# Kernel tuning notes

Measured on AMD Instinct MI355X. Metric: run time of the kernel, lower is better.

Reference implementation:

```python
import jax, jax.numpy as jnp
import numpy as np

B, T, H, NEX, ED = 65536, 20, 10, 13, 3

def _p(k, shape):
    return (jax.random.normal(k, shape, jnp.float32) * 0.1)

def setup_inputs() -> dict:
    key = jax.random.key(0)
    ks = jax.random.split(key, 24)
    e = jax.random.randint(ks[0], (B, T), 0, NEX, dtype=jnp.int32)
    f = jax.random.normal(ks[1], (B, T, 3), jnp.float32)
    emb = _p(ks[2], (NEX, ED)).at[0].set(0.0)  # row 0 zeroed as in torch init
    feat_w = _p(ks[3], (3, 3))
    feat_b = _p(ks[4], (3,))
    d = {"e": e, "f": f, "emb": emb, "feat_w": feat_w, "feat_b": feat_b}
    i = 5
    for layer, insz in ((0, 6), (1, 2 * H)):
        for sfx in ("", "r"):
            d[f"w_ih_l{layer}{sfx}"] = _p(ks[i], (4 * H, insz)); i += 1
            d[f"w_hh_l{layer}{sfx}"] = _p(ks[i], (4 * H, H)); i += 1
            d[f"b_ih_l{layer}{sfx}"] = _p(ks[i], (4 * H,)); i += 1
            d[f"b_hh_l{layer}{sfx}"] = _p(ks[i], (4 * H,)); i += 1
    return d

def _lstm_dir(x, w_ih, w_hh, b_ih, b_hh, reverse):
    # x: (B, T, I) -> hidden sequence (B, T, H). PyTorch gate order: i, f, g, o.
    xs = jnp.swapaxes(x, 0, 1)                      # (T, B, I)
    pre = xs @ w_ih.T + (b_ih + b_hh)               # input contribution, (T, B, 4H)
    def step(carry, p):
        h, c = carry
        g = p + h @ w_hh.T
        i, fg, gg, o = jnp.split(g, 4, axis=-1)
        c = jax.nn.sigmoid(fg) * c + jax.nn.sigmoid(i) * jnp.tanh(gg)
        h = jax.nn.sigmoid(o) * jnp.tanh(c)
        return (h, c), h
    nb = x.shape[0]
    init = (jnp.zeros((nb, H), x.dtype), jnp.zeros((nb, H), x.dtype))
    _, hs = jax.lax.scan(step, init, pre, reverse=reverse)
    return jnp.swapaxes(hs, 0, 1)                   # (B, T, H)

def _bilstm_layer(x, pf, pb):
    hf = _lstm_dir(x, *pf, reverse=False)
    hb = _lstm_dir(x, *pb, reverse=True)
    return jnp.concatenate([hf, hb], axis=-1)       # (B, T, 2H)

def reference(e, f, emb, feat_w, feat_b,
              w_ih_l0, w_hh_l0, b_ih_l0, b_hh_l0,
              w_ih_l0r, w_hh_l0r, b_ih_l0r, b_hh_l0r,
              w_ih_l1, w_hh_l1, b_ih_l1, b_hh_l1,
              w_ih_l1r, w_hh_l1r, b_ih_l1r, b_hh_l1r):
    ev = emb[e]                                     # (B, T, 3)
    f3 = f.reshape(-1, T, 3)
    mask = (f3[:, :, 1] != 0).astype(f.dtype)       # (B, T)
    fv = f3 @ feat_w.T + feat_b                     # (B, T, 3)
    x = jnp.concatenate([ev, fv], axis=2)           # (B, T, 6)
    x = _bilstm_layer(x, (w_ih_l0, w_hh_l0, b_ih_l0, b_hh_l0),
                         (w_ih_l0r, w_hh_l0r, b_ih_l0r, b_hh_l0r))
    x = _bilstm_layer(x, (w_ih_l1, w_hh_l1, b_ih_l1, b_hh_l1),
                         (w_ih_l1r, w_hh_l1r, b_ih_l1r, b_hh_l1r))
    ipe = jax.nn.relu(x[:, :, -1] * mask)           # last channel = backward dir unit H-1
    total = ipe.sum(axis=1, keepdims=True)          # (B, 1)
    return (total, ipe)
```

## Files before the change

### kernel.cpp

```cpp
#include <hip/hip_runtime.h>

#define BB 65536
#define TT 20
#define NBLK 2048

#define WS_WGT 0
#define WS_HF0 4096
#define PK1 0x00003C00u

#define LOG2E  1.442695041f
#define LOG2E2 2.885390082f

typedef unsigned u32;
typedef __fp16 f16x8 __attribute__((ext_vector_type(8)));
typedef float   f32x16 __attribute__((ext_vector_type(16)));
typedef u32     u32x4 __attribute__((ext_vector_type(4)));
typedef __fp16  h2v   __attribute__((ext_vector_type(2)));

__device__ __forceinline__ u32 pk_h16(float a, float b) {
    h2v v = __builtin_amdgcn_cvt_pkrtz(a, b);
    return __builtin_bit_cast(u32, v);
}
__device__ __forceinline__ f32x16 MFMA(u32x4 a, u32x4 b, f32x16 c) {
    return __builtin_amdgcn_mfma_f32_32x32x16_f16(
        __builtin_bit_cast(f16x8, a), __builtin_bit_cast(f16x8, b), c, 0, 0, 0);
}

__device__ __forceinline__ void unit_cr(float ai, float af, float ag, float ao,
                                        float* c, float* h) {
    float pi = __builtin_amdgcn_exp2f(-LOG2E * ai);
    float pf = __builtin_amdgcn_exp2f(-LOG2E * af);
    float q  = __builtin_amdgcn_exp2f(LOG2E2 * ag);
    float fv = __builtin_amdgcn_rcpf(1.0f + pf);
    float ig = (q - 1.0f) * __builtin_amdgcn_rcpf((1.0f + pi) * (q + 1.0f));
    float cv = fmaf(fv, *c, ig);
    *c = cv;
    float po = __builtin_amdgcn_exp2f(-LOG2E * ao);
    float qc = __builtin_amdgcn_exp2f(LOG2E2 * cv);
    *h = (qc - 1.0f) * __builtin_amdgcn_rcpf((1.0f + po) * (qc + 1.0f));
}

__device__ __forceinline__ u32x4 pack_h(const float* h, bool hi, int xaddr, u32 b3) {
    u32 send = hi ? pk_h16(h[3], h[4]) : __float_as_uint(h[4]);
    u32 recv = (u32)__builtin_amdgcn_ds_bpermute(xaddr, (int)send);
    u32 lo0 = pk_h16(h[0], h[1]), lo1 = pk_h16(h[2], h[3]);
    u32 hi0 = pk_h16(__uint_as_float(recv), h[0]);
    u32 hi1 = pk_h16(h[1], h[2]);
    u32x4 b;
    b[0] = hi ? hi0 : lo0;
    b[1] = hi ? hi1 : lo1;
    b[2] = hi ? 0u : recv;
    b[3] = b3;
    return b;
}

__device__ __forceinline__ void cell_update5(const f32x16 a0, const f32x16 a1,
                                             float* c, float* h) {
#pragma unroll
    for (int v = 0; v < 4; ++v)
        unit_cr(a0[v], a0[4 + v], a0[8 + v], a0[12 + v], &c[v], &h[v]);
    unit_cr(a1[0], a1[1], a1[2], a1[3], &c[4], &h[4]);
}

__device__ __forceinline__ int inv_pi(int row) {
    if (row < 32) { int q = row >> 3, rem = row & 7; return q * 10 + 5 * (rem >> 2) + (rem & 3); }
    if (row < 40) { int lo = row - 32; return (lo & 3) * 10 + 5 * (lo >> 2) + 4; }
    return -1;
}

__global__ __launch_bounds__(256)
void prep_mfma(
    const float* __restrict__ wih0, const float* __restrict__ whh0,
    const float* __restrict__ bih0, const float* __restrict__ bhh0,
    const float* __restrict__ wih0r,const float* __restrict__ whh0r,
    const float* __restrict__ bih0r,const float* __restrict__ bhh0r,
    const float* __restrict__ wih1r,const float* __restrict__ whh1r,
    const float* __restrict__ bih1r,const float* __restrict__ bhh1r,
    u32* __restrict__ ws)
{
    for (int gid = threadIdx.x; gid < 14 * 64 * 4; gid += 256) {
        int fid = gid >> 8, l = (gid >> 2) & 63, j = gid & 3;
        int g = l >> 5;
        int tile, chunk;
        if (fid < 8) { tile = (fid >> 1) & 1; chunk = fid & 1; }
        else         { int q = fid - 8; tile = q / 3; chunk = q % 3; }
        int row = tile * 32 + (l & 31);
        int orow = inv_pi(row);
        int kb = (j >> 1) * 8 + 4 * g + (j & 1) * 2;
        float v[2] = {0.f, 0.f};
        if (orow >= 0) {
#pragma unroll
            for (int s = 0; s < 2; ++s) {
                int k = kb + s;
                float val = 0.f;
                if (fid < 8) {
                    bool bwd = fid >= 4;
                    if (chunk == 0) {
                        if (k < 6)       val = (bwd ? wih0r : wih0)[orow * 6 + k];
                        else if (k == 6) val = (bwd ? bih0r[orow] + bhh0r[orow]
                                                    : bih0[orow] + bhh0[orow]);
                    } else {
                        if (k < 10)      val = (bwd ? whh0r : whh0)[orow * 10 + k];
                    }
                } else {
                    if (chunk == 0)      { if (k < 10) val = wih1r[orow * 20 + k]; }
                    else if (chunk == 1) { if (k < 10) val = wih1r[orow * 20 + 10 + k]; }
                    else {
                        if (k < 10)      val = whh1r[orow * 10 + k];
                        else if (k == 10) val = bih1r[orow] + bhh1r[orow];
                    }
                }
                v[s] = val;
            }
        }
        ws[WS_WGT + (fid * 64 + l) * 4 + j] = pk_h16(v[0], v[1]);
    }
}

template<bool WS> struct Lds {
    u32   x[TT][3][32];
    float m[TT][32];
    u32   hf[WS ? 1 : TT][160];
};

template<bool WS>
__global__ __launch_bounds__(64)
void bilstm_mfma(
    const int*   __restrict__ eidx, const float* __restrict__ f,
    const float* __restrict__ emb,  const float* __restrict__ fw,
    const float* __restrict__ fb,
    const u32* __restrict__ wsr, u32* __restrict__ ghf,
    float* __restrict__ out)
{
    __shared__ Lds<WS> lds;
    const int  lane = threadIdx.x;
    const int  e    = lane & 31;
    const bool hi   = lane >= 32;
    const int  wid  = blockIdx.x;
    const int  b0   = wid * 32;
    const int  xaddr = (lane ^ 32) << 2;
    u32* hfp = ghf + (size_t)wid * TT * 160;

    {
        float fw0=fw[0],fw1=fw[1],fw2=fw[2],fw3=fw[3],fw4=fw[4];
        float fw5=fw[5],fw6=fw[6],fw7=fw[7],fw8=fw[8];
        float fb0=fb[0],fb1=fb[1],fb2=fb[2];
#pragma unroll 1
        for (int it = 0; it < 10; ++it) {
            int idx = lane + it * 64;
            int ee = idx / 20, t = idx - ee * 20;
            int gi = (b0 + ee) * TT + t;
            float f0 = f[gi * 3], f1 = f[gi * 3 + 1], f2v = f[gi * 3 + 2];
            int ei = eidx[gi] * 3;
            float x0 = emb[ei], x1 = emb[ei + 1], x2 = emb[ei + 2];
            float x3 = fmaf(fw0, f0, fmaf(fw1, f1, fmaf(fw2, f2v, fb0)));
            float x4 = fmaf(fw3, f0, fmaf(fw4, f1, fmaf(fw5, f2v, fb1)));
            float x5 = fmaf(fw6, f0, fmaf(fw7, f1, fmaf(fw8, f2v, fb2)));
            lds.x[t][0][ee] = pk_h16(x0, x1);
            lds.x[t][1][ee] = pk_h16(x2, x3);
            lds.x[t][2][ee] = pk_h16(x4, x5);
            lds.m[t][ee]    = (f1 != 0.f) ? 1.f : 0.f;
        }
    }

    const u32x4* wv = (const u32x4*)wsr;
    const f32x16 zf = {};

    {
        u32x4 wf0 = wv[0 * 64 + lane], wf1 = wv[1 * 64 + lane];
        u32x4 wf2 = wv[2 * 64 + lane], wf3 = wv[3 * 64 + lane];
        float cf[5] = {0,0,0,0,0}, hv[5] = {0,0,0,0,0};
        u32x4 bx0;
        {
            u32 x01 = lds.x[0][0][e], x23 = lds.x[0][1][e], x45 = lds.x[0][2][e];
            bx0[0] = hi ? x45 : x01; bx0[1] = hi ? PK1 : x23; bx0[2] = 0u; bx0[3] = 0u;
        }
        f32x16 a0x = MFMA(wf0, bx0, zf);
        f32x16 a1x = MFMA(wf2, bx0, zf);
#pragma unroll 1
        for (int t = 0; t < TT; ++t) {
            u32x4 bh = pack_h(hv, hi, xaddr, 0u);
            f32x16 a0 = MFMA(wf1, bh, a0x);
            f32x16 a1 = MFMA(wf3, bh, a1x);
            if (t + 1 < TT) {
                u32 x01 = lds.x[t+1][0][e], x23 = lds.x[t+1][1][e], x45 = lds.x[t+1][2][e];
                u32x4 bx; bx[0] = hi ? x45 : x01; bx[1] = hi ? PK1 : x23; bx[2] = 0u; bx[3] = 0u;
                a0x = MFMA(wf0, bx, zf);
                a1x = MFMA(wf2, bx, zf);
            }
            cell_update5(a0, a1, cf, hv);
            u32x4 st = pack_h(hv, hi, xaddr, 0u);
            if (WS) {
                *(uint2*)(hfp + t * 160 + lane * 2) = make_uint2(st[0], st[1]);
                if (!hi) hfp[t * 160 + 128 + e] = st[2];
            } else {
                lds.hf[t][lane * 2] = st[0]; lds.hf[t][lane * 2 + 1] = st[1];
                if (!hi) lds.hf[t][128 + e] = st[2];
            }
        }
    }

    {
        u32x4 wb0 = wv[4 * 64 + lane], wb1 = wv[5 * 64 + lane];
        u32x4 wb2 = wv[6 * 64 + lane], wb3 = wv[7 * 64 + lane];
        u32x4 wB0 = wv[8 * 64 + lane], wB1 = wv[9 * 64 + lane], wB2 = wv[10 * 64 + lane];
        u32x4 wB3 = wv[11 * 64 + lane], wB4 = wv[12 * 64 + lane], wB5 = wv[13 * 64 + lane];
        float cb[5] = {0,0,0,0,0}, hbv[5] = {0,0,0,0,0};
        float cc[5] = {0,0,0,0,0}, h1v[5] = {0,0,0,0,0};
        float tot = 0.f;

        {
            u32 x01 = lds.x[TT-1][0][e], x23 = lds.x[TT-1][1][e], x45 = lds.x[TT-1][2][e];
            u32x4 bx; bx[0] = hi ? x45 : x01; bx[1] = hi ? PK1 : x23; bx[2] = 0u; bx[3] = 0u;
            f32x16 a0 = MFMA(wb0, bx, zf);
            f32x16 a1 = MFMA(wb2, bx, zf);
            cell_update5(a0, a1, cb, hbv);
        }
        uint2 cur2; u32 curw;
        if (WS) { cur2 = *(const uint2*)(hfp + (TT-1) * 160 + lane * 2);
                  curw = hfp[(TT-1) * 160 + 128 + e]; }
        else    { cur2 = make_uint2(lds.hf[TT-1][lane * 2], lds.hf[TT-1][lane * 2 + 1]);
                  curw = lds.hf[TT-1][128 + e]; }

#pragma unroll 1
        for (int t = TT - 1; t >= 1; --t) {
            uint2 nxt2; u32 nxtw;
            if (WS) { nxt2 = *(const uint2*)(hfp + (t-1) * 160 + lane * 2);
                      nxtw = hfp[(t-1) * 160 + 128 + e]; }
            else    { nxt2 = make_uint2(lds.hf[t-1][lane * 2], lds.hf[t-1][lane * 2 + 1]);
                      nxtw = lds.hf[t-1][128 + e]; }
            u32x4 shared = pack_h(hbv, hi, xaddr, 0u);
            u32x4 bh1    = pack_h(h1v, hi, xaddr, hi ? 0u : PK1);
            u32x4 bhf; bhf[0] = cur2.x; bhf[1] = cur2.y; bhf[2] = hi ? 0u : curw; bhf[3] = 0u;
            f32x16 B0 = MFMA(wB0, bhf, zf); B0 = MFMA(wB1, shared, B0); B0 = MFMA(wB2, bh1, B0);
            f32x16 B1 = MFMA(wB3, bhf, zf); B1 = MFMA(wB4, shared, B1); B1 = MFMA(wB5, bh1, B1);
            u32 x01 = lds.x[t-1][0][e], x23 = lds.x[t-1][1][e], x45 = lds.x[t-1][2][e];
            u32x4 bx; bx[0] = hi ? x45 : x01; bx[1] = hi ? PK1 : x23; bx[2] = 0u; bx[3] = 0u;
            f32x16 A0 = MFMA(wb0, bx, zf); A0 = MFMA(wb1, shared, A0);
            f32x16 A1 = MFMA(wb2, bx, zf); A1 = MFMA(wb3, shared, A1);
            cell_update5(B0, B1, cc, h1v);
            if (hi) {
                float ip = fmaxf(h1v[4] * lds.m[t][e], 0.f);
                out[BB + (b0 + e) * TT + t] = ip;
                tot += ip;
            }
            cell_update5(A0, A1, cb, hbv);
            cur2 = nxt2; curw = nxtw;
        }
        {
            u32x4 shared = pack_h(hbv, hi, xaddr, 0u);
            u32x4 bh1    = pack_h(h1v, hi, xaddr, hi ? 0u : PK1);
            u32x4 bhf; bhf[0] = cur2.x; bhf[1] = cur2.y; bhf[2] = hi ? 0u : curw; bhf[3] = 0u;
            f32x16 B0 = MFMA(wB0, bhf, zf); B0 = MFMA(wB1, shared, B0); B0 = MFMA(wB2, bh1, B0);
            f32x16 B1 = MFMA(wB3, bhf, zf); B1 = MFMA(wB4, shared, B1); B1 = MFMA(wB5, bh1, B1);
            cell_update5(B0, B1, cc, h1v);
            if (hi) {
                float ip = fmaxf(h1v[4] * lds.m[0][e], 0.f);
                out[BB + (b0 + e) * TT + 0] = ip;
                tot += ip;
                out[b0 + e] = tot;
            }
        }
    }
}

extern "C" void kernel_launch(void* const* d_in, const int* in_sizes, int n_in,
                              void* d_out, int out_size, void* d_ws, size_t ws_size,
                              hipStream_t stream) {
    const int*   eidx  = (const int*)  d_in[0];
    const float* f     = (const float*)d_in[1];
    const float* emb   = (const float*)d_in[2];
    const float* fw    = (const float*)d_in[3];
    const float* fb    = (const float*)d_in[4];
    const float* wih0  = (const float*)d_in[5];
    const float* whh0  = (const float*)d_in[6];
    const float* bih0  = (const float*)d_in[7];
    const float* bhh0  = (const float*)d_in[8];
    const float* wih0r = (const float*)d_in[9];
    const float* whh0r = (const float*)d_in[10];
    const float* bih0r = (const float*)d_in[11];
    const float* bhh0r = (const float*)d_in[12];
    const float* wih1r = (const float*)d_in[17];
    const float* whh1r = (const float*)d_in[18];
    const float* bih1r = (const float*)d_in[19];
    const float* bhh1r = (const float*)d_in[20];
    float* out = (float*)d_out;
    u32* ws = (u32*)d_ws;

    hipLaunchKernelGGL(prep_mfma, dim3(1), dim3(256), 0, stream,
                       wih0, whh0, bih0, bhh0, wih0r, whh0r, bih0r, bhh0r,
                       wih1r, whh1r, bih1r, bhh1r, ws);

    const size_t need = (size_t)(WS_HF0 + (size_t)NBLK * TT * 160) * 4;
    dim3 grid(NBLK), block(64);
    if (ws_size >= need) {
        hipLaunchKernelGGL(bilstm_mfma<true>, grid, block, 0, stream,
                           eidx, f, emb, fw, fb, ws, ws + WS_HF0, out);
    } else {
        hipLaunchKernelGGL(bilstm_mfma<false>, grid, block, 0, stream,
                           eidx, f, emb, fw, fb, ws, ws + WS_HF0, out);
    }
}
```

Baseline: 69.94 us.

## Split bidirectional layer 0 into parallel per-direction blocks plus a layer-1 kernel

Layer 0 moves into its own kernel that runs forward and backward directions as separate workgroups (4096 blocks), each writing its hidden-state fragments to workspace. A second kernel then runs the layer-1 backward recurrence by reading both direction buffers. The aim is to double parallelism and shorten the serial dependency chain per block, because the backward layer-0 recurrence no longer sits in the same loop as layer 1. The cost is an extra launch, duplicated input preprocessing, and more global memory traffic for the layer-0 backward states. The first step also skips the MFMA with a zero hidden state.

```diff
diff --git a/kernel.cpp b/kernel.cpp
--- a/kernel.cpp
+++ b/kernel.cpp
@@ -2,10 +2,13 @@
 
 #define BB 65536
 #define TT 20
-#define NBLK 2048
+#define NE 2048
+#define FRAG_T 160
 
 #define WS_WGT 0
 #define WS_HF0 4096
+#define WS_HB0 (WS_HF0 + NE * TT * FRAG_T)
+#define WS_END (WS_HB0 + NE * TT * FRAG_T)
 #define PK1 0x00003C00u
 
 #define LOG2E  1.442695041f
@@ -117,10 +120,137 @@
     }
 }
 
+__global__ __launch_bounds__(64)
+void bilstm_l0(
+    const int*   __restrict__ eidx, const float* __restrict__ f,
+    const float* __restrict__ emb,  const float* __restrict__ fw,
+    const float* __restrict__ fb,
+    const u32* __restrict__ wsr, u32* __restrict__ ghf, u32* __restrict__ ghb)
+{
+    __shared__ u32 xs[TT][3][32];
+    const int  lane = threadIdx.x;
+    const int  e    = lane & 31;
+    const bool hi   = lane >= 32;
+    const int  wid  = blockIdx.x;
+    const int  dir  = wid >> 11;
+    const int  eb   = wid & (NE - 1);
+    const int  b0   = eb * 32;
+    const int  xaddr = (lane ^ 32) << 2;
+
+    {
+        float fw0=fw[0],fw1=fw[1],fw2=fw[2],fw3=fw[3],fw4=fw[4];
+        float fw5=fw[5],fw6=fw[6],fw7=fw[7],fw8=fw[8];
+        float fb0=fb[0],fb1=fb[1],fb2=fb[2];
+#pragma unroll 1
+        for (int it = 0; it < 10; ++it) {
+            int idx = lane + it * 64;
+            int ee = idx / 20, t = idx - ee * 20;
+            int gi = (b0 + ee) * TT + t;
+            float f0 = f[gi * 3], f1 = f[gi * 3 + 1], f2v = f[gi * 3 + 2];
+            int ei = eidx[gi] * 3;
+            float x0 = emb[ei], x1 = emb[ei + 1], x2 = emb[ei + 2];
+            float x3 = fmaf(fw0, f0, fmaf(fw1, f1, fmaf(fw2, f2v, fb0)));
+            float x4 = fmaf(fw3, f0, fmaf(fw4, f1, fmaf(fw5, f2v, fb1)));
+            float x5 = fmaf(fw6, f0, fmaf(fw7, f1, fmaf(fw8, f2v, fb2)));
+            xs[t][0][ee] = pk_h16(x0, x1);
+            xs[t][1][ee] = pk_h16(x2, x3);
+            xs[t][2][ee] = pk_h16(x4, x5);
+        }
+    }
+
+    const u32x4* wv = (const u32x4*)wsr;
+    const f32x16 zf = {};
+    u32* outp = (dir ? ghb : ghf) + (size_t)eb * TT * FRAG_T;
+    const int wbase = dir ? 4 : 0;
+    u32x4 w0 = wv[(wbase + 0) * 64 + lane], w1 = wv[(wbase + 1) * 64 + lane];
+    u32x4 w2 = wv[(wbase + 2) * 64 + lane], w3 = wv[(wbase + 3) * 64 + lane];
+
+    auto BX = [&](int t) {
+        u32 x01 = xs[t][0][e], x23 = xs[t][1][e], x45 = xs[t][2][e];
+        u32x4 b; b[0] = hi ? x45 : x01; b[1] = hi ? PK1 : x23; b[2] = 0u; b[3] = 0u;
+        return b;
+    };
+
+    float cst[5] = {0,0,0,0,0}, hv[5] = {0,0,0,0,0};
+    const int t0 = dir ? TT - 1 : 0;
+    const int dt = dir ? -1 : 1;
+    f32x16 a0x = MFMA(w0, BX(t0), zf);
+    f32x16 a1x = MFMA(w2, BX(t0), zf);
+    u32x4 bh;
+#pragma unroll 1
+    for (int s = 0; s < TT; ++s) {
+        const int t = t0 + s * dt;
+        f32x16 a0 = a0x, a1 = a1x;
+        if (s > 0) { a0 = MFMA(w1, bh, a0); a1 = MFMA(w3, bh, a1); }
+        if (s + 1 < TT) {
+            u32x4 bx = BX(t + dt);
+            a0x = MFMA(w0, bx, zf);
+            a1x = MFMA(w2, bx, zf);
+        }
+        cell_update5(a0, a1, cst, hv);
+        bh = pack_h(hv, hi, xaddr, 0u);
+        *(uint2*)(outp + t * FRAG_T + lane * 2) = make_uint2(bh[0], bh[1]);
+        if (!hi) outp[t * FRAG_T + 128 + e] = bh[2];
+    }
+}
+
+__global__ __launch_bounds__(64)
+void bilstm_cb(
+    const float* __restrict__ f, const u32* __restrict__ wsr,
+    const u32* __restrict__ ghf, const u32* __restrict__ ghb,
+    float* __restrict__ out)
+{
+    const int  lane = threadIdx.x;
+    const int  e    = lane & 31;
+    const bool hi   = lane >= 32;
+    const int  eb   = blockIdx.x;
+    const int  b0   = eb * 32;
+    const int  xaddr = (lane ^ 32) << 2;
+    const u32x4* wv = (const u32x4*)wsr;
+    u32x4 wB0 = wv[8 * 64 + lane],  wB1 = wv[9 * 64 + lane],  wB2 = wv[10 * 64 + lane];
+    u32x4 wB3 = wv[11 * 64 + lane], wB4 = wv[12 * 64 + lane], wB5 = wv[13 * 64 + lane];
+    const u32* hfp = ghf + (size_t)eb * TT * FRAG_T;
+    const u32* hbp = ghb + (size_t)eb * TT * FRAG_T;
+    const f32x16 zf = {};
+    float cc[5] = {0,0,0,0,0}, h1v[5] = {0,0,0,0,0}, tot = 0.f;
+
+    uint2 hf2 = *(const uint2*)(hfp + (TT - 1) * FRAG_T + lane * 2);
+    u32   hfw = hfp[(TT - 1) * FRAG_T + 128 + e];
+    uint2 hb2 = *(const uint2*)(hbp + (TT - 1) * FRAG_T + lane * 2);
+    u32   hbw = hbp[(TT - 1) * FRAG_T + 128 + e];
+    float f1v = f[((b0 + e) * TT + (TT - 1)) * 3 + 1];
+
+#pragma unroll 1
+    for (int t = TT - 1; t >= 0; --t) {
+        u32x4 bhf; bhf[0] = hf2.x; bhf[1] = hf2.y; bhf[2] = hi ? 0u : hfw; bhf[3] = 0u;
+        u32x4 bhb; bhb[0] = hb2.x; bhb[1] = hb2.y; bhb[2] = hi ? 0u : hbw; bhb[3] = 0u;
+        f32x16 B0 = MFMA(wB0, bhf, zf); B0 = MFMA(wB1, bhb, B0);
+        f32x16 B1 = MFMA(wB3, bhf, zf); B1 = MFMA(wB4, bhb, B1);
+        float fcur = f1v;
+        if (t > 0) {
+            hf2 = *(const uint2*)(hfp + (t - 1) * FRAG_T + lane * 2);
+            hfw = hfp[(t - 1) * FRAG_T + 128 + e];
+            hb2 = *(const uint2*)(hbp + (t - 1) * FRAG_T + lane * 2);
+            hbw = hbp[(t - 1) * FRAG_T + 128 + e];
+            f1v = f[((b0 + e) * TT + (t - 1)) * 3 + 1];
+        }
+        u32x4 bh1 = pack_h(h1v, hi, xaddr, hi ? 0u : PK1);
+        B0 = MFMA(wB2, bh1, B0);
+        B1 = MFMA(wB5, bh1, B1);
+        cell_update5(B0, B1, cc, h1v);
+        if (hi) {
+            float ip = fmaxf(h1v[4] * (fcur != 0.f ? 1.f : 0.f), 0.f);
+            out[BB + (b0 + e) * TT + t] = ip;
+            tot += ip;
+        }
+    }
+    if (hi) out[b0 + e] = tot;
+}
+
 template<bool WS> struct Lds {
     u32   x[TT][3][32];
     float m[TT][32];
-    u32   hf[WS ? 1 : TT][160];
+    u32   hf[WS ? 1 : TT][FRAG_T];
 };
 
 template<bool WS>
@@ -139,7 +269,7 @@
     const int  wid  = blockIdx.x;
     const int  b0   = wid * 32;
     const int  xaddr = (lane ^ 32) << 2;
-    u32* hfp = ghf + (size_t)wid * TT * 160;
+    u32* hfp = ghf + (size_t)wid * TT * FRAG_T;
 
     {
         float fw0=fw[0],fw1=fw[1],fw2=fw[2],fw3=fw[3],fw4=fw[4];
@@ -165,7 +295,6 @@
 
     const u32x4* wv = (const u32x4*)wsr;
     const f32x16 zf = {};
-
     {
         u32x4 wf0 = wv[0 * 64 + lane], wf1 = wv[1 * 64 + lane];
         u32x4 wf2 = wv[2 * 64 + lane], wf3 = wv[3 * 64 + lane];
@@ -177,11 +306,11 @@
         }
         f32x16 a0x = MFMA(wf0, bx0, zf);
         f32x16 a1x = MFMA(wf2, bx0, zf);
+        u32x4 bh;
 #pragma unroll 1
         for (int t = 0; t < TT; ++t) {
-            u32x4 bh = pack_h(hv, hi, xaddr, 0u);
-            f32x16 a0 = MFMA(wf1, bh, a0x);
-            f32x16 a1 = MFMA(wf3, bh, a1x);
+            f32x16 a0 = a0x, a1 = a1x;
+            if (t > 0) { a0 = MFMA(wf1, bh, a0); a1 = MFMA(wf3, bh, a1); }
             if (t + 1 < TT) {
                 u32 x01 = lds.x[t+1][0][e], x23 = lds.x[t+1][1][e], x45 = lds.x[t+1][2][e];
                 u32x4 bx; bx[0] = hi ? x45 : x01; bx[1] = hi ? PK1 : x23; bx[2] = 0u; bx[3] = 0u;
@@ -189,17 +318,16 @@
                 a1x = MFMA(wf2, bx, zf);
             }
             cell_update5(a0, a1, cf, hv);
-            u32x4 st = pack_h(hv, hi, xaddr, 0u);
+            bh = pack_h(hv, hi, xaddr, 0u);
             if (WS) {
-                *(uint2*)(hfp + t * 160 + lane * 2) = make_uint2(st[0], st[1]);
-                if (!hi) hfp[t * 160 + 128 + e] = st[2];
+                *(uint2*)(hfp + t * FRAG_T + lane * 2) = make_uint2(bh[0], bh[1]);
+                if (!hi) hfp[t * FRAG_T + 128 + e] = bh[2];
             } else {
-                lds.hf[t][lane * 2] = st[0]; lds.hf[t][lane * 2 + 1] = st[1];
-                if (!hi) lds.hf[t][128 + e] = st[2];
+                lds.hf[t][lane * 2] = bh[0]; lds.hf[t][lane * 2 + 1] = bh[1];
+                if (!hi) lds.hf[t][128 + e] = bh[2];
             }
         }
     }
-
     {
         u32x4 wb0 = wv[4 * 64 + lane], wb1 = wv[5 * 64 + lane];
         u32x4 wb2 = wv[6 * 64 + lane], wb3 = wv[7 * 64 + lane];
@@ -208,7 +336,6 @@
         float cb[5] = {0,0,0,0,0}, hbv[5] = {0,0,0,0,0};
         float cc[5] = {0,0,0,0,0}, h1v[5] = {0,0,0,0,0};
         float tot = 0.f;
-
         {
             u32 x01 = lds.x[TT-1][0][e], x23 = lds.x[TT-1][1][e], x45 = lds.x[TT-1][2][e];
             u32x4 bx; bx[0] = hi ? x45 : x01; bx[1] = hi ? PK1 : x23; bx[2] = 0u; bx[3] = 0u;
@@ -217,16 +344,15 @@
             cell_update5(a0, a1, cb, hbv);
         }
         uint2 cur2; u32 curw;
-        if (WS) { cur2 = *(const uint2*)(hfp + (TT-1) * 160 + lane * 2);
-                  curw = hfp[(TT-1) * 160 + 128 + e]; }
+        if (WS) { cur2 = *(const uint2*)(hfp + (TT-1) * FRAG_T + lane * 2);
+                  curw = hfp[(TT-1) * FRAG_T + 128 + e]; }
         else    { cur2 = make_uint2(lds.hf[TT-1][lane * 2], lds.hf[TT-1][lane * 2 + 1]);
                   curw = lds.hf[TT-1][128 + e]; }
-
 #pragma unroll 1
         for (int t = TT - 1; t >= 1; --t) {
             uint2 nxt2; u32 nxtw;
-            if (WS) { nxt2 = *(const uint2*)(hfp + (t-1) * 160 + lane * 2);
-                      nxtw = hfp[(t-1) * 160 + 128 + e]; }
+            if (WS) { nxt2 = *(const uint2*)(hfp + (t-1) * FRAG_T + lane * 2);
+                      nxtw = hfp[(t-1) * FRAG_T + 128 + e]; }
             else    { nxt2 = make_uint2(lds.hf[t-1][lane * 2], lds.hf[t-1][lane * 2 + 1]);
                       nxtw = lds.hf[t-1][128 + e]; }
             u32x4 shared = pack_h(hbv, hi, xaddr, 0u);
@@ -291,13 +417,18 @@
                        wih0, whh0, bih0, bhh0, wih0r, whh0r, bih0r, bhh0r,
                        wih1r, whh1r, bih1r, bhh1r, ws);
 
-    const size_t need = (size_t)(WS_HF0 + (size_t)NBLK * TT * 160) * 4;
-    dim3 grid(NBLK), block(64);
-    if (ws_size >= need) {
-        hipLaunchKernelGGL(bilstm_mfma<true>, grid, block, 0, stream,
+    const size_t need_split = (size_t)WS_END * 4;
+    const size_t need_r9    = (size_t)(WS_HF0 + (size_t)NE * TT * FRAG_T) * 4;
+    if (ws_size >= need_split) {
+        hipLaunchKernelGGL(bilstm_l0, dim3(2 * NE), dim3(64), 0, stream,
+                           eidx, f, emb, fw, fb, ws, ws + WS_HF0, ws + WS_HB0);
+        hipLaunchKernelGGL(bilstm_cb, dim3(NE), dim3(64), 0, stream,
+                           f, ws, ws + WS_HF0, ws + WS_HB0, out);
+    } else if (ws_size >= need_r9) {
+        hipLaunchKernelGGL(bilstm_mfma<true>, dim3(NE), dim3(64), 0, stream,
                            eidx, f, emb, fw, fb, ws, ws + WS_HF0, out);
     } else {
-        hipLaunchKernelGGL(bilstm_mfma<false>, grid, block, 0, stream,
+        hipLaunchKernelGGL(bilstm_mfma<false>, dim3(NE), dim3(64), 0, stream,
                            eidx, f, emb, fw, fb, ws, ws + WS_HF0, out);
     }
 }
```

Result: slower. 78.66 us (+12.5%).

## Switch BiLSTM to 16x16x32 MFMA with 16 sequences per wave

Applied to the files above, without the earlier changes.

Replaces the 32x32x16 MFMA kernel (32 sequences per 64-thread block) with a new kernel using 16x16x32 MFMA tiles. Each wave handles 16 sequences and a block holds four waves. Input and recurrent weights are packed into one K=32 operand, so the x and h contributions come from a single MFMA, and h is exchanged through LDS with explicit waitcnt fences instead of bpermute packing. Layer 0 runs the forward and backward directions interleaved in one loop, then layer 1's backward pass reads the stored hidden states. This aims to cut wasted MFMA work on the padded 32-row tiles and raise occupancy, at the cost of an LDS round-trip and fence on every step.

```diff
diff --git a/kernel.cpp b/kernel.cpp
--- a/kernel.cpp
+++ b/kernel.cpp
@@ -2,18 +2,24 @@
 
 #define BB 65536
 #define TT 20
-#define NBLK 2048
-
-#define WS_WGT 0
-#define WS_HF0 4096
-#define PK1 0x00003C00u
+#define NG16 4096
+#define FR_ROW 160
+
+#define WS_AF  0
+#define WS_OLD 2304
+#define WS_FR  8192
+#define PKB 0x00003C00u
 
 #define LOG2E  1.442695041f
 #define LOG2E2 2.885390082f
+
+#define LDS_FENCE() do { asm volatile("s_waitcnt lgkmcnt(0)" ::: "memory"); \
+                         __builtin_amdgcn_sched_barrier(0); } while (0)
 
 typedef unsigned u32;
 typedef __fp16 f16x8 __attribute__((ext_vector_type(8)));
 typedef float   f32x16 __attribute__((ext_vector_type(16)));
+typedef float   f32x4v __attribute__((ext_vector_type(4)));
 typedef u32     u32x4 __attribute__((ext_vector_type(4)));
 typedef __fp16  h2v   __attribute__((ext_vector_type(2)));
 
@@ -21,7 +27,11 @@
     h2v v = __builtin_amdgcn_cvt_pkrtz(a, b);
     return __builtin_bit_cast(u32, v);
 }
-__device__ __forceinline__ f32x16 MFMA(u32x4 a, u32x4 b, f32x16 c) {
+__device__ __forceinline__ f32x4v MFMA16(u32x4 a, u32x4 b, f32x4v c) {
+    return __builtin_amdgcn_mfma_f32_16x16x32_f16(
+        __builtin_bit_cast(f16x8, a), __builtin_bit_cast(f16x8, b), c, 0, 0, 0);
+}
+__device__ __forceinline__ f32x16 MFMA32(u32x4 a, u32x4 b, f32x16 c) {
     return __builtin_amdgcn_mfma_f32_32x32x16_f16(
         __builtin_bit_cast(f16x8, a), __builtin_bit_cast(f16x8, b), c, 0, 0, 0);
 }
@@ -40,20 +50,209 @@
     *h = (qc - 1.0f) * __builtin_amdgcn_rcpf((1.0f + po) * (qc + 1.0f));
 }
 
-__device__ __forceinline__ u32x4 pack_h(const float* h, bool hi, int xaddr, u32 b3) {
+__global__ __launch_bounds__(256)
+void prep16(
+    const float* __restrict__ wih0, const float* __restrict__ whh0,
+    const float* __restrict__ bih0, const float* __restrict__ bhh0,
+    const float* __restrict__ wih0r,const float* __restrict__ whh0r,
+    const float* __restrict__ bih0r,const float* __restrict__ bhh0r,
+    const float* __restrict__ wih1r,const float* __restrict__ whh1r,
+    const float* __restrict__ bih1r,const float* __restrict__ bhh1r,
+    u32* __restrict__ ws)
+{
+    for (int gid = threadIdx.x; gid < 9 * 64 * 4; gid += 256) {
+        int fid = gid >> 8;
+        int ct = fid / 3, T = fid % 3;
+        int l = (gid >> 2) & 63, j = gid & 3;
+        int m = l & 15, qq = l >> 4;
+        int unit = T * 4 + (m >> 2), gate = m & 3;
+        float v[2] = {0.f, 0.f};
+        if (unit <= 9) {
+            int orow = gate * 10 + unit;
+#pragma unroll
+            for (int s = 0; s < 2; ++s) {
+                int k = (j >> 1) * 16 + 4 * qq + (j & 1) * 2 + s;
+                float val = 0.f;
+                if (ct < 2) {
+                    const float* wih = ct ? wih0r : wih0;
+                    const float* whh = ct ? whh0r : whh0;
+                    if (k < 6)            val = wih[orow * 6 + k];
+                    else if (k == 6)      val = ct ? (bih0r[orow] + bhh0r[orow])
+                                               : (bih0[orow] + bhh0[orow]);
+                    else if (k >= 8 && k <= 17) val = whh[orow * 10 + (k - 8)];
+                } else {
+                    if (k < 20)           val = wih1r[orow * 20 + k];
+                    else if (k <= 29)     val = whh1r[orow * 10 + (k - 20)];
+                    else if (k == 30)     val = bih1r[orow] + bhh1r[orow];
+                }
+                v[s] = val;
+            }
+        }
+        ws[WS_AF + (fid * 64 + l) * 4 + j] = pk_h16(v[0], v[1]);
+    }
+}
+
+struct Lds16 {
+    uint2 bx[4][TT][16][2];
+    float m[4][TT][16];
+    unsigned short hx[4][2][16][12];
+    u32   zpad[2];
+};
+
+__global__ __launch_bounds__(256, 4)
+void bilstm16(
+    const int*   __restrict__ eidx, const float* __restrict__ f,
+    const float* __restrict__ emb,  const float* __restrict__ fw,
+    const float* __restrict__ fb,
+    const u32* __restrict__ wsr, u32* __restrict__ fr,
+    float* __restrict__ out)
+{
+    __shared__ Lds16 lds;
+    const int tid  = threadIdx.x;
+    const int lane = tid & 63;
+    const int e    = lane & 15;
+    const int q    = lane >> 4;
+    const int wv   = __builtin_amdgcn_readfirstlane(tid >> 6);
+    const int g    = blockIdx.x * 4 + wv;
+    const int b0   = g * 16;
+    const int be   = e * 24;
+    u32* frp = fr + (size_t)g * TT * FR_ROW;
+
+    {
+        float fw0=fw[0],fw1=fw[1],fw2=fw[2],fw3=fw[3],fw4=fw[4];
+        float fw5=fw[5],fw6=fw[6],fw7=fw[7],fw8=fw[8];
+        float fb0=fb[0],fb1=fb[1],fb2=fb[2];
+#pragma unroll 1
+        for (int it = 0; it < 5; ++it) {
+            int idx = lane + it * 64;
+            int ee = idx / TT, t = idx - ee * TT;
+            int gi = (b0 + ee) * TT + t;
+            float f0 = f[gi * 3], f1 = f[gi * 3 + 1], f2v = f[gi * 3 + 2];
+            int ei = eidx[gi] * 3;
+            float x0 = emb[ei], x1 = emb[ei + 1], x2 = emb[ei + 2];
+            float x3 = fmaf(fw0, f0, fmaf(fw1, f1, fmaf(fw2, f2v, fb0)));
+            float x4 = fmaf(fw3, f0, fmaf(fw4, f1, fmaf(fw5, f2v, fb1)));
+            float x5 = fmaf(fw6, f0, fmaf(fw7, f1, fmaf(fw8, f2v, fb2)));
+            lds.bx[wv][t][ee][0] = make_uint2(pk_h16(x0, x1), pk_h16(x2, x3));
+            lds.bx[wv][t][ee][1] = make_uint2(pk_h16(x4, x5), PKB);
+            lds.m[wv][t][ee]     = (f1 != 0.f) ? 1.f : 0.f;
+        }
+        u32* zz = (u32*)&lds.hx[wv][0][0][0];
+        zz[lane] = 0u; zz[lane + 64] = 0u; zz[lane + 128] = 0u;
+        if (lane < 2) lds.zpad[lane] = 0u;
+    }
+    LDS_FENCE();
+
+    char* bxb  = (char*)&lds.bx[wv][0][e][0];
+    char* hxFb = (char*)&lds.hx[wv][0][0][0];
+    char* hxBb = (char*)&lds.hx[wv][1][0][0];
+    char* hxF  = hxFb + be;
+    char* hxB  = hxBb + be;
+    char* zp   = (char*)lds.zpad;
+    const int uw0 = be + 2 * q, uw1 = be + 8 + 2 * q, uw2 = be + 16 + 2 * q;
+
+    const u32x4* wv4 = (const u32x4*)(wsr + WS_AF);
+    const f32x4v z4 = {};
+
+    {
+        u32x4 F0 = wv4[0 * 64 + lane], F1 = wv4[1 * 64 + lane], F2 = wv4[2 * 64 + lane];
+        u32x4 G0 = wv4[3 * 64 + lane], G1 = wv4[4 * 64 + lane], G2 = wv4[5 * 64 + lane];
+        const char* aF  = (q < 2) ? (bxb + q * 8) : (hxF + (q - 2) * 8);
+        const char* aB  = (q < 2) ? (bxb + q * 8 + 19 * 256) : (hxB + (q - 2) * 8);
+        const char* a2F = (q == 0) ? (hxF + 16) : zp;
+        const char* a2B = (q == 0) ? (hxB + 16) : zp;
+        const int   strA = (q < 2) ? 256 : 0;
+
+        float cF[3] = {0,0,0}, cB[3] = {0,0,0};
+#pragma unroll 1
+        for (int s = 0; s < TT; ++s) {
+            uint2 uF = *(const uint2*)(aF + s * strA);
+            u32   wF = *(const u32*)a2F;
+            u32x4 bf; bf[0] = uF.x; bf[1] = uF.y; bf[2] = wF; bf[3] = 0u;
+            f32x4v A0 = MFMA16(F0, bf, z4), A1 = MFMA16(F1, bf, z4), A2 = MFMA16(F2, bf, z4);
+            uint2 uB = *(const uint2*)(aB - s * strA);
+            u32   wB = *(const u32*)a2B;
+            u32x4 bb; bb[0] = uB.x; bb[1] = uB.y; bb[2] = wB; bb[3] = 0u;
+            f32x4v C0 = MFMA16(G0, bb, z4), C1 = MFMA16(G1, bb, z4), C2 = MFMA16(G2, bb, z4);
+            float hF[3], hB[3];
+            unit_cr(A0[0], A0[1], A0[2], A0[3], &cF[0], &hF[0]);
+            unit_cr(A1[0], A1[1], A1[2], A1[3], &cF[1], &hF[1]);
+            unit_cr(A2[0], A2[1], A2[2], A2[3], &cF[2], &hF[2]);
+            unit_cr(C0[0], C0[1], C0[2], C0[3], &cB[0], &hB[0]);
+            unit_cr(C1[0], C1[1], C1[2], C1[3], &cB[1], &hB[1]);
+            unit_cr(C2[0], C2[1], C2[2], C2[3], &cB[2], &hB[2]);
+            *(__fp16*)(hxFb + uw0) = (__fp16)hF[0];
+            *(__fp16*)(hxFb + uw1) = (__fp16)hF[1];
+            *(__fp16*)(hxFb + uw2) = (__fp16)hF[2];
+            *(__fp16*)(hxBb + uw0) = (__fp16)hB[0];
+            *(__fp16*)(hxBb + uw1) = (__fp16)hB[1];
+            *(__fp16*)(hxBb + uw2) = (__fp16)hB[2];
+            LDS_FENCE();
+            u32* frT = frp + s * FR_ROW;
+            u32* frB = frp + (TT - 1 - s) * FR_ROW;
+            frT[e * 10 + q]     = *(u32*)(hxF + q * 4);
+            frB[e * 10 + 5 + q] = *(u32*)(hxB + q * 4);
+            if (q == 0) {
+                frT[e * 10 + 4] = *(u32*)(hxF + 16);
+                frB[e * 10 + 9] = *(u32*)(hxB + 16);
+            }
+        }
+    }
+
+    {
+        u32x4 H0 = wv4[6 * 64 + lane], H1 = wv4[7 * 64 + lane], H2 = wv4[8 * 64 + lane];
+        u32* hz = (u32*)hxFb;
+        hz[lane] = 0u;
+        if (lane < 32) hz[64 + lane] = 0u;
+        LDS_FENCE();
+        const char* caddr = (q == 0) ? zp : (hxF + (q - 1) * 8);
+        const int loffA = e * 10 + q * 2;
+        const int loffB = e * 10 + 8;
+        float cH[3] = {0,0,0}, tot = 0.f;
+        uint2 La = *(const uint2*)(frp + (TT - 1) * FR_ROW + loffA);
+        uint2 Lb = *(const uint2*)(frp + (TT - 1) * FR_ROW + loffB);
+#pragma unroll 1
+        for (int t = TT - 1; t >= 0; --t) {
+            uint2 C = *(const uint2*)caddr;
+            u32x4 bc;
+            bc[0] = La.x;
+            bc[1] = La.y;
+            bc[2] = (q == 0) ? Lb.x : C.x;
+            bc[3] = (q == 0) ? Lb.y : ((q == 3) ? PKB : C.y);
+            if (t > 0) {
+                La = *(const uint2*)(frp + (t - 1) * FR_ROW + loffA);
+                Lb = *(const uint2*)(frp + (t - 1) * FR_ROW + loffB);
+            }
+            f32x4v D0 = MFMA16(H0, bc, z4), D1 = MFMA16(H1, bc, z4), D2 = MFMA16(H2, bc, z4);
+            float hH[3];
+            unit_cr(D0[0], D0[1], D0[2], D0[3], &cH[0], &hH[0]);
+            unit_cr(D1[0], D1[1], D1[2], D1[3], &cH[1], &hH[1]);
+            unit_cr(D2[0], D2[1], D2[2], D2[3], &cH[2], &hH[2]);
+            *(__fp16*)(hxFb + uw0) = (__fp16)hH[0];
+            *(__fp16*)(hxFb + uw1) = (__fp16)hH[1];
+            *(__fp16*)(hxFb + uw2) = (__fp16)hH[2];
+            LDS_FENCE();
+            if (q == 1) {
+                float ip = fmaxf(hH[2] * lds.m[wv][t][e], 0.f);
+                out[BB + (b0 + e) * TT + t] = ip;
+                tot += ip;
+            }
+        }
+        if (q == 1) out[b0 + e] = tot;
+    }
+}
+
+__device__ __forceinline__ u32x4 pack_h32(const float* h, bool hi, int xaddr, u32 b3) {
     u32 send = hi ? pk_h16(h[3], h[4]) : __float_as_uint(h[4]);
     u32 recv = (u32)__builtin_amdgcn_ds_bpermute(xaddr, (int)send);
     u32 lo0 = pk_h16(h[0], h[1]), lo1 = pk_h16(h[2], h[3]);
     u32 hi0 = pk_h16(__uint_as_float(recv), h[0]);
     u32 hi1 = pk_h16(h[1], h[2]);
     u32x4 b;
-    b[0] = hi ? hi0 : lo0;
-    b[1] = hi ? hi1 : lo1;
-    b[2] = hi ? 0u : recv;
-    b[3] = b3;
+    b[0] = hi ? hi0 : lo0; b[1] = hi ? hi1 : lo1;
+    b[2] = hi ? 0u : recv; b[3] = b3;
     return b;
 }
-
 __device__ __forceinline__ void cell_update5(const f32x16 a0, const f32x16 a1,
                                              float* c, float* h) {
 #pragma unroll
@@ -61,15 +260,13 @@
         unit_cr(a0[v], a0[4 + v], a0[8 + v], a0[12 + v], &c[v], &h[v]);
     unit_cr(a1[0], a1[1], a1[2], a1[3], &c[4], &h[4]);
 }
-
 __device__ __forceinline__ int inv_pi(int row) {
     if (row < 32) { int q = row >> 3, rem = row & 7; return q * 10 + 5 * (rem >> 2) + (rem & 3); }
     if (row < 40) { int lo = row - 32; return (lo & 3) * 10 + 5 * (lo >> 2) + 4; }
     return -1;
 }
-
 __global__ __launch_bounds__(256)
-void prep_mfma(
+void prep_old(
     const float* __restrict__ wih0, const float* __restrict__ whh0,
     const float* __restrict__ bih0, const float* __restrict__ bhh0,
     const float* __restrict__ wih0r,const float* __restrict__ whh0r,
@@ -80,13 +277,13 @@
 {
     for (int gid = threadIdx.x; gid < 14 * 64 * 4; gid += 256) {
         int fid = gid >> 8, l = (gid >> 2) & 63, j = gid & 3;
-        int g = l >> 5;
+        int gq = l >> 5;
         int tile, chunk;
         if (fid < 8) { tile = (fid >> 1) & 1; chunk = fid & 1; }
-        else         { int q = fid - 8; tile = q / 3; chunk = q % 3; }
+        else         { int q2 = fid - 8; tile = q2 / 3; chunk = q2 % 3; }
         int row = tile * 32 + (l & 31);
         int orow = inv_pi(row);
-        int kb = (j >> 1) * 8 + 4 * g + (j & 1) * 2;
+        int kb = (j >> 1) * 8 + 4 * gq + (j & 1) * 2;
         float v[2] = {0.f, 0.f};
         if (orow >= 0) {
 #pragma unroll
@@ -99,48 +296,36 @@
                         if (k < 6)       val = (bwd ? wih0r : wih0)[orow * 6 + k];
                         else if (k == 6) val = (bwd ? bih0r[orow] + bhh0r[orow]
                                                     : bih0[orow] + bhh0[orow]);
-                    } else {
-                        if (k < 10)      val = (bwd ? whh0r : whh0)[orow * 10 + k];
-                    }
+                    } else { if (k < 10) val = (bwd ? whh0r : whh0)[orow * 10 + k]; }
                 } else {
                     if (chunk == 0)      { if (k < 10) val = wih1r[orow * 20 + k]; }
                     else if (chunk == 1) { if (k < 10) val = wih1r[orow * 20 + 10 + k]; }
                     else {
-                        if (k < 10)      val = whh1r[orow * 10 + k];
+                        if (k < 10)       val = whh1r[orow * 10 + k];
                         else if (k == 10) val = bih1r[orow] + bhh1r[orow];
                     }
                 }
                 v[s] = val;
             }
         }
-        ws[WS_WGT + (fid * 64 + l) * 4 + j] = pk_h16(v[0], v[1]);
-    }
-}
-
-template<bool WS> struct Lds {
-    u32   x[TT][3][32];
-    float m[TT][32];
-    u32   hf[WS ? 1 : TT][160];
-};
-
-template<bool WS>
+        ws[WS_OLD + (fid * 64 + l) * 4 + j] = pk_h16(v[0], v[1]);
+    }
+}
+struct LdsFB { u32 x[TT][3][32]; float m[TT][32]; u32 hf[TT][160]; };
 __global__ __launch_bounds__(64)
-void bilstm_mfma(
+void bilstm_fb(
     const int*   __restrict__ eidx, const float* __restrict__ f,
     const float* __restrict__ emb,  const float* __restrict__ fw,
     const float* __restrict__ fb,
-    const u32* __restrict__ wsr, u32* __restrict__ ghf,
-    float* __restrict__ out)
+    const u32* __restrict__ wsr, float* __restrict__ out)
 {
-    __shared__ Lds<WS> lds;
+    __shared__ LdsFB lds;
     const int  lane = threadIdx.x;
     const int  e    = lane & 31;
     const bool hi   = lane >= 32;
     const int  wid  = blockIdx.x;
     const int  b0   = wid * 32;
     const int  xaddr = (lane ^ 32) << 2;
-    u32* hfp = ghf + (size_t)wid * TT * 160;
-
     {
         float fw0=fw[0],fw1=fw[1],fw2=fw[2],fw3=fw[3],fw4=fw[4];
         float fw5=fw[5],fw6=fw[6],fw7=fw[7],fw8=fw[8];
@@ -162,10 +347,8 @@
             lds.m[t][ee]    = (f1 != 0.f) ? 1.f : 0.f;
         }
     }
-
-    const u32x4* wv = (const u32x4*)wsr;
+    const u32x4* wv = (const u32x4*)(wsr + WS_OLD);
     const f32x16 zf = {};
-
     {
         u32x4 wf0 = wv[0 * 64 + lane], wf1 = wv[1 * 64 + lane];
         u32x4 wf2 = wv[2 * 64 + lane], wf3 = wv[3 * 64 + lane];
@@ -173,33 +356,27 @@
         u32x4 bx0;
         {
             u32 x01 = lds.x[0][0][e], x23 = lds.x[0][1][e], x45 = lds.x[0][2][e];
-            bx0[0] = hi ? x45 : x01; bx0[1] = hi ? PK1 : x23; bx0[2] = 0u; bx0[3] = 0u;
-        }
-        f32x16 a0x = MFMA(wf0, bx0, zf);
-        f32x16 a1x = MFMA(wf2, bx0, zf);
+            bx0[0] = hi ? x45 : x01; bx0[1] = hi ? PKB : x23; bx0[2] = 0u; bx0[3] = 0u;
+        }
+        f32x16 a0x = MFMA32(wf0, bx0, zf);
+        f32x16 a1x = MFMA32(wf2, bx0, zf);
+        u32x4 bh;
 #pragma unroll 1
         for (int t = 0; t < TT; ++t) {
-            u32x4 bh = pack_h(hv, hi, xaddr, 0u);
-            f32x16 a0 = MFMA(wf1, bh, a0x);
-            f32x16 a1 = MFMA(wf3, bh, a1x);
+            f32x16 a0 = a0x, a1 = a1x;
+            if (t > 0) { a0 = MFMA32(wf1, bh, a0); a1 = MFMA32(wf3, bh, a1); }
             if (t + 1 < TT) {
                 u32 x01 = lds.x[t+1][0][e], x23 = lds.x[t+1][1][e], x45 = lds.x[t+1][2][e];
-                u32x4 bx; bx[0] = hi ? x45 : x01; bx[1] = hi ? PK1 : x23; bx[2] = 0u; bx[3] = 0u;
-                a0x = MFMA(wf0, bx, zf);
-                a1x = MFMA(wf2, bx, zf);
+                u32x4 bx; bx[0] = hi ? x45 : x01; bx[1] = hi ? PKB : x23; bx[2] = 0u; bx[3] = 0u;
+                a0x = MFMA32(wf0, bx, zf);
+                a1x = MFMA32(wf2, bx, zf);
             }
             cell_update5(a0, a1, cf, hv);
-            u32x4 st = pack_h(hv, hi, xaddr, 0u);
-            if (WS) {
-                *(uint2*)(hfp + t * 160 + lane * 2) = make_uint2(st[0], st[1]);
-                if (!hi) hfp[t * 160 + 128 + e] = st[2];
-            } else {
-                lds.hf[t][lane * 2] = st[0]; lds.hf[t][lane * 2 + 1] = st[1];
-                if (!hi) lds.hf[t][128 + e] = st[2];
-            }
-        }
-    }
-
+            bh = pack_h32(hv, hi, xaddr, 0u);
+            lds.hf[t][lane * 2] = bh[0]; lds.hf[t][lane * 2 + 1] = bh[1];
+            if (!hi) lds.hf[t][128 + e] = bh[2];
+        }
+    }
     {
         u32x4 wb0 = wv[4 * 64 + lane], wb1 = wv[5 * 64 + lane];
         u32x4 wb2 = wv[6 * 64 + lane], wb3 = wv[7 * 64 + lane];
@@ -208,36 +385,28 @@
         float cb[5] = {0,0,0,0,0}, hbv[5] = {0,0,0,0,0};
         float cc[5] = {0,0,0,0,0}, h1v[5] = {0,0,0,0,0};
         float tot = 0.f;
-
         {
             u32 x01 = lds.x[TT-1][0][e], x23 = lds.x[TT-1][1][e], x45 = lds.x[TT-1][2][e];
-            u32x4 bx; bx[0] = hi ? x45 : x01; bx[1] = hi ? PK1 : x23; bx[2] = 0u; bx[3] = 0u;
-            f32x16 a0 = MFMA(wb0, bx, zf);
-            f32x16 a1 = MFMA(wb2, bx, zf);
+            u32x4 bx; bx[0] = hi ? x45 : x01; bx[1] = hi ? PKB : x23; bx[2] = 0u; bx[3] = 0u;
+            f32x16 a0 = MFMA32(wb0, bx, zf);
+            f32x16 a1 = MFMA32(wb2, bx, zf);
             cell_update5(a0, a1, cb, hbv);
         }
-        uint2 cur2; u32 curw;
-        if (WS) { cur2 = *(const uint2*)(hfp + (TT-1) * 160 + lane * 2);
-                  curw = hfp[(TT-1) * 160 + 128 + e]; }
-        else    { cur2 = make_uint2(lds.hf[TT-1][lane * 2], lds.hf[TT-1][lane * 2 + 1]);
-                  curw = lds.hf[TT-1][128 + e]; }
-
+        uint2 cur2 = make_uint2(lds.hf[TT-1][lane * 2], lds.hf[TT-1][lane * 2 + 1]);
+        u32   curw = lds.hf[TT-1][128 + e];
 #pragma unroll 1
         for (int t = TT - 1; t >= 1; --t) {
-            uint2 nxt2; u32 nxtw;
-            if (WS) { nxt2 = *(const uint2*)(hfp + (t-1) * 160 + lane * 2);
-                      nxtw = hfp[(t-1) * 160 + 128 + e]; }
-            else    { nxt2 = make_uint2(lds.hf[t-1][lane * 2], lds.hf[t-1][lane * 2 + 1]);
-                      nxtw = lds.hf[t-1][128 + e]; }
-            u32x4 shared = pack_h(hbv, hi, xaddr, 0u);
-            u32x4 bh1    = pack_h(h1v, hi, xaddr, hi ? 0u : PK1);
+            uint2 nxt2 = make_uint2(lds.hf[t-1][lane * 2], lds.hf[t-1][lane * 2 + 1]);
+            u32   nxtw = lds.hf[t-1][128 + e];
+            u32x4 shared = pack_h32(hbv, hi, xaddr, 0u);
+            u32x4 bh1    = pack_h32(h1v, hi, xaddr, hi ? 0u : PKB);
             u32x4 bhf; bhf[0] = cur2.x; bhf[1] = cur2.y; bhf[2] = hi ? 0u : curw; bhf[3] = 0u;
-            f32x16 B0 = MFMA(wB0, bhf, zf); B0 = MFMA(wB1, shared, B0); B0 = MFMA(wB2, bh1, B0);
-            f32x16 B1 = MFMA(wB3, bhf, zf); B1 = MFMA(wB4, shared, B1); B1 = MFMA(wB5, bh1, B1);
+            f32x16 B0 = MFMA32(wB0, bhf, zf); B0 = MFMA32(wB1, shared, B0); B0 = MFMA32(wB2, bh1, B0);
+            f32x16 B1 = MFMA32(wB3, bhf, zf); B1 = MFMA32(wB4, shared, B1); B1 = MFMA32(wB5, bh1, B1);
             u32 x01 = lds.x[t-1][0][e], x23 = lds.x[t-1][1][e], x45 = lds.x[t-1][2][e];
-            u32x4 bx; bx[0] = hi ? x45 : x01; bx[1] = hi ? PK1 : x23; bx[2] = 0u; bx[3] = 0u;
-            f32x16 A0 = MFMA(wb0, bx, zf); A0 = MFMA(wb1, shared, A0);
-            f32x16 A1 = MFMA(wb2, bx, zf); A1 = MFMA(wb3, shared, A1);
+            u32x4 bx; bx[0] = hi ? x45 : x01; bx[1] = hi ? PKB : x23; bx[2] = 0u; bx[3] = 0u;
+            f32x16 A0 = MFMA32(wb0, bx, zf); A0 = MFMA32(wb1, shared, A0);
+            f32x16 A1 = MFMA32(wb2, bx, zf); A1 = MFMA32(wb3, shared, A1);
             cell_update5(B0, B1, cc, h1v);
             if (hi) {
                 float ip = fmaxf(h1v[4] * lds.m[t][e], 0.f);
@@ -248,11 +417,11 @@
             cur2 = nxt2; curw = nxtw;
         }
         {
-            u32x4 shared = pack_h(hbv, hi, xaddr, 0u);
-            u32x4 bh1    = pack_h(h1v, hi, xaddr, hi ? 0u : PK1);
+            u32x4 shared = pack_h32(hbv, hi, xaddr, 0u);
+            u32x4 bh1    = pack_h32(h1v, hi, xaddr, hi ? 0u : PKB);
             u32x4 bhf; bhf[0] = cur2.x; bhf[1] = cur2.y; bhf[2] = hi ? 0u : curw; bhf[3] = 0u;
-            f32x16 B0 = MFMA(wB0, bhf, zf); B0 = MFMA(wB1, shared, B0); B0 = MFMA(wB2, bh1, B0);
-            f32x16 B1 = MFMA(wB3, bhf, zf); B1 = MFMA(wB4, shared, B1); B1 = MFMA(wB5, bh1, B1);
+            f32x16 B0 = MFMA32(wB0, bhf, zf); B0 = MFMA32(wB1, shared, B0); B0 = MFMA32(wB2, bh1, B0);
+            f32x16 B1 = MFMA32(wB3, bhf, zf); B1 = MFMA32(wB4, shared, B1); B1 = MFMA32(wB5, bh1, B1);
             cell_update5(B0, B1, cc, h1v);
             if (hi) {
                 float ip = fmaxf(h1v[4] * lds.m[0][e], 0.f);
@@ -287,17 +456,18 @@
     float* out = (float*)d_out;
     u32* ws = (u32*)d_ws;
 
-    hipLaunchKernelGGL(prep_mfma, dim3(1), dim3(256), 0, stream,
-                       wih0, whh0, bih0, bhh0, wih0r, whh0r, bih0r, bhh0r,
-                       wih1r, whh1r, bih1r, bhh1r, ws);
-
-    const size_t need = (size_t)(WS_HF0 + (size_t)NBLK * TT * 160) * 4;
-    dim3 grid(NBLK), block(64);
-    if (ws_size >= need) {
-        hipLaunchKernelGGL(bilstm_mfma<true>, grid, block, 0, stream,
-                           eidx, f, emb, fw, fb, ws, ws + WS_HF0, out);
+    const size_t need16 = (size_t)(WS_FR + (size_t)NG16 * TT * FR_ROW + 64) * 4;
+    if (ws_size >= need16) {
+        hipLaunchKernelGGL(prep16, dim3(1), dim3(256), 0, stream,
+                           wih0, whh0, bih0, bhh0, wih0r, whh0r, bih0r, bhh0r,
+                           wih1r, whh1r, bih1r, bhh1r, ws);
+        hipLaunchKernelGGL(bilstm16, dim3(NG16 / 4), dim3(256), 0, stream,
+                           eidx, f, emb, fw, fb, ws, ws + WS_FR, out);
     } else {
-        hipLaunchKernelGGL(bilstm_mfma<false>, grid, block, 0, stream,
-                           eidx, f, emb, fw, fb, ws, ws + WS_HF0, out);
-    }
-}
+        hipLaunchKernelGGL(prep_old, dim3(1), dim3(256), 0, stream,
+                           wih0, whh0, bih0, bhh0, wih0r, whh0r, bih0r, bhh0r,
+                           wih1r, whh1r, bih1r, bhh1r, ws);
+        hipLaunchKernelGGL(bilstm_fb, dim3(BB / 32), dim3(64), 0, stream,
+                           eidx, f, emb, fw, fb, ws, out);
+    }
+}
```

Result: slower. 73.23 us (+4.7%).
